# Kernel optimization log

Hardware: AMD Instinct MI355X
Metric: run time of the kernel (lower is better)

## Reference

```python
import jax, jax.numpy as jnp
import numpy as np


def setup_inputs() -> dict:
    key = jax.random.key(0)
    x = jax.random.normal(key, (128, 256, 32, 32), dtype=jnp.float32)
    return {"x": x, "topk": 5}


def reference(x, topk):
    B = x.shape[0]
    flat = x.reshape(B, -1)                      # [B, N]
    _, idx = jax.lax.top_k(flat, topk)           # [B, k] indices into N
    out = jnp.zeros_like(flat)
    out = out.at[jnp.arange(B)[:, None], idx].set(1.0)
    return out.reshape(x.shape)
```

## Files before the change

### kernel.cpp

```cpp
#include <hip/hip_runtime.h>
#include <limits.h>
#include <math.h>
#include <stdint.h>

#define BROWS 128
#define NCOLS (256 * 32 * 32)
#define K 5
#define BPR 16
#define TPB 256
#define CHUNK (NCOLS / BPR)
#define F4T (CHUNK / 4 / TPB)
#define CAP 256

typedef float v4f __attribute__((ext_vector_type(4)));

__device__ __forceinline__ uint64_t make_key(float f, uint32_t idx) {
    uint32_t u = __float_as_uint(f);
    u = (u & 0x80000000u) ? ~u : (u | 0x80000000u);
    return ((uint64_t)u << 32) | (uint32_t)(~idx);
}
__device__ __forceinline__ uint32_t key_idx(uint64_t k) { return ~(uint32_t)k; }

#define KEY_NEG_INF 0x007FFFFF00000000ULL

__device__ __forceinline__ void insert5(uint64_t (&key)[K], uint64_t c) {
    if (c > key[K - 1]) {
        key[K - 1] = c;
#pragma unroll
        for (int s = K - 1; s > 0; --s) {
            if (key[s] > key[s - 1]) {
                uint64_t t = key[s]; key[s] = key[s - 1]; key[s - 1] = t;
            }
        }
    }
}

__device__ __forceinline__ void wave_reduce5(uint64_t (&key)[K]) {
#pragma unroll
    for (int off = 1; off < 64; off <<= 1) {
        uint64_t ok[K];
#pragma unroll
        for (int k = 0; k < K; ++k)
            ok[k] = __shfl_xor((unsigned long long)key[k], off, 64);
#pragma unroll
        for (int k = 0; k < K; ++k) insert5(key, ok[k]);
    }
}

__device__ __forceinline__ void insert5f(float (&v)[K], float c) {
    if (c > v[K - 1]) {
        v[K - 1] = c;
#pragma unroll
        for (int s = K - 1; s > 0; --s) {
            if (v[s] > v[s - 1]) { float t = v[s]; v[s] = v[s - 1]; v[s - 1] = t; }
        }
    }
}

__global__ __launch_bounds__(TPB) void wta_gmax(const float* __restrict__ x,
                                                float* __restrict__ gmax) {
    const int gb = blockIdx.x;
    const float4* __restrict__ x4 = (const float4*)(x + (size_t)gb * CHUNK);
    const int t = threadIdx.x;

    float m = -INFINITY;
#pragma unroll
    for (int i = 0; i < F4T; ++i) {
        const float4 d = x4[t + i * TPB];
        m = fmaxf(m, fmaxf(fmaxf(d.x, d.y), fmaxf(d.z, d.w)));
    }
#pragma unroll
    for (int off = 1; off < 64; off <<= 1)
        m = fmaxf(m, __shfl_xor(m, off, 64));

    __shared__ float sm[TPB / 64];
    if ((t & 63) == 0) sm[t >> 6] = m;
    __syncthreads();
    if (t == 0)
        gmax[gb] = fmaxf(fmaxf(sm[0], sm[1]), fmaxf(sm[2], sm[3]));
}

__global__ __launch_bounds__(64) void wta_thresh(const float* __restrict__ gmax,
                                                 float* __restrict__ T,
                                                 int* __restrict__ cnt) {
    const int row = blockIdx.x, lane = threadIdx.x;
    float v[K];
#pragma unroll
    for (int k = 0; k < K; ++k) v[k] = -INFINITY;
    if (lane < BPR) insert5f(v, gmax[row * BPR + lane]);
#pragma unroll
    for (int off = 1; off < 64; off <<= 1) {
        float ov[K];
#pragma unroll
        for (int k = 0; k < K; ++k) ov[k] = __shfl_xor(v[k], off, 64);
#pragma unroll
        for (int k = 0; k < K; ++k) insert5f(v, ov[k]);
    }
    if (lane == 0) { T[row] = v[K - 1]; cnt[row] = 0; }
}

__global__ __launch_bounds__(TPB) void wta_fillfilter(const float* __restrict__ x,
                                                      float* __restrict__ out,
                                                      const float* __restrict__ T,
                                                      int* __restrict__ cnt,
                                                      uint64_t* __restrict__ cand) {
    const int gb  = blockIdx.x;
    const int row = gb / BPR;
    const int blk = gb % BPR;
    const size_t base = (size_t)gb * CHUNK;
    const float4* __restrict__ x4 = (const float4*)(x + base);
    v4f* __restrict__ o4 = (v4f*)(out + base);
    const int t = threadIdx.x;
    const float Trow = T[row];
    const v4f z = {0.f, 0.f, 0.f, 0.f};

#pragma unroll
    for (int h = 0; h < 2; ++h) {
        float4 r[F4T / 2];
#pragma unroll
        for (int j = 0; j < F4T / 2; ++j)
            r[j] = x4[t + (h * (F4T / 2) + j) * TPB];
#pragma unroll
        for (int j = 0; j < F4T / 2; ++j)
            __builtin_nontemporal_store(z, &o4[t + (h * (F4T / 2) + j) * TPB]);
#pragma unroll
        for (int j = 0; j < F4T / 2; ++j) {
            const float4 d = r[j];
            const float m = fmaxf(fmaxf(d.x, d.y), fmaxf(d.z, d.w));
            if (m >= Trow) {
                const uint32_t e = (uint32_t)blk * CHUNK +
                                   (uint32_t)(t + (h * (F4T / 2) + j) * TPB) * 4u;
                const float vs[4] = {d.x, d.y, d.z, d.w};
#pragma unroll
                for (int c = 0; c < 4; ++c) {
                    if (vs[c] >= Trow) {
                        const int slot = atomicAdd(&cnt[row], 1);
                        if (slot < CAP) cand[row * CAP + slot] = make_key(vs[c], e + c);
                    }
                }
            }
        }
    }
}

__global__ __launch_bounds__(64) void wta_final(const int* __restrict__ cnt,
                                                const uint64_t* __restrict__ cand,
                                                float* __restrict__ out) {
    const int row = blockIdx.x, lane = threadIdx.x;
    const int n = min(cnt[row], CAP);

    uint64_t key[K];
#pragma unroll
    for (int k = 0; k < K; ++k) key[k] = KEY_NEG_INF;
    for (int c = lane; c < n; c += 64) insert5(key, cand[row * CAP + c]);

    wave_reduce5(key);

    if (lane == 0) {
#pragma unroll
        for (int k = 0; k < K; ++k)
            if (key[k] != KEY_NEG_INF)
                out[(size_t)row * NCOLS + key_idx(key[k])] = 1.0f;
    }
}

extern "C" void kernel_launch(void* const* d_in, const int* in_sizes, int n_in,
                              void* d_out, int out_size, void* d_ws, size_t ws_size,
                              hipStream_t stream) {
    const float* x = (const float*)d_in[0];
    float* out = (float*)d_out;

    uint64_t* cand = (uint64_t*)d_ws;
    float* gmax = (float*)(cand + (size_t)BROWS * CAP);
    float* T    = gmax + BROWS * BPR;
    int*   cnt  = (int*)(T + BROWS);

    wta_gmax<<<BROWS * BPR, TPB, 0, stream>>>(x, gmax);
    wta_thresh<<<BROWS, 64, 0, stream>>>(gmax, T, cnt);
    wta_fillfilter<<<BROWS * BPR, TPB, 0, stream>>>(x, out, T, cnt, cand);
    wta_final<<<BROWS, 64, 0, stream>>>(cnt, cand, out);
}
```

Measured before the change: 252.7 us.

## Fuse max prepass into single streaming pass with per-block top-k candidates

Removes the separate global-max and threshold kernels so x is read once instead of twice. Each thread keeps a running top-5 of packed value/index keys and uses its 5th value as a skip threshold. The block reduces this to its own top-5 via wave shuffles and shared memory, and a final kernel merges the 16 per-block lists per row. This trades the atomic candidate buffer for more per-thread insertion work early in the scan.

```diff
diff --git a/kernel.cpp b/kernel.cpp
--- a/kernel.cpp
+++ b/kernel.cpp
@@ -10,7 +10,7 @@
 #define TPB 256
 #define CHUNK (NCOLS / BPR)
 #define F4T (CHUNK / 4 / TPB)
-#define CAP 256
+#define NW (TPB / 64)
 
 typedef float v4f __attribute__((ext_vector_type(4)));
 
@@ -20,6 +20,11 @@
     return ((uint64_t)u << 32) | (uint32_t)(~idx);
 }
 __device__ __forceinline__ uint32_t key_idx(uint64_t k) { return ~(uint32_t)k; }
+__device__ __forceinline__ float key_val(uint64_t k) {
+    uint32_t u = (uint32_t)(k >> 32);
+    u = (u & 0x80000000u) ? (u & 0x7FFFFFFFu) : ~u;
+    return __uint_as_float(u);
+}
 
 #define KEY_NEG_INF 0x007FFFFF00000000ULL
 
@@ -47,63 +52,9 @@
     }
 }
 
-__device__ __forceinline__ void insert5f(float (&v)[K], float c) {
-    if (c > v[K - 1]) {
-        v[K - 1] = c;
-#pragma unroll
-        for (int s = K - 1; s > 0; --s) {
-            if (v[s] > v[s - 1]) { float t = v[s]; v[s] = v[s - 1]; v[s - 1] = t; }
-        }
-    }
-}
-
-__global__ __launch_bounds__(TPB) void wta_gmax(const float* __restrict__ x,
-                                                float* __restrict__ gmax) {
-    const int gb = blockIdx.x;
-    const float4* __restrict__ x4 = (const float4*)(x + (size_t)gb * CHUNK);
-    const int t = threadIdx.x;
-
-    float m = -INFINITY;
-#pragma unroll
-    for (int i = 0; i < F4T; ++i) {
-        const float4 d = x4[t + i * TPB];
-        m = fmaxf(m, fmaxf(fmaxf(d.x, d.y), fmaxf(d.z, d.w)));
-    }
-#pragma unroll
-    for (int off = 1; off < 64; off <<= 1)
-        m = fmaxf(m, __shfl_xor(m, off, 64));
-
-    __shared__ float sm[TPB / 64];
-    if ((t & 63) == 0) sm[t >> 6] = m;
-    __syncthreads();
-    if (t == 0)
-        gmax[gb] = fmaxf(fmaxf(sm[0], sm[1]), fmaxf(sm[2], sm[3]));
-}
-
-__global__ __launch_bounds__(64) void wta_thresh(const float* __restrict__ gmax,
-                                                 float* __restrict__ T,
-                                                 int* __restrict__ cnt) {
-    const int row = blockIdx.x, lane = threadIdx.x;
-    float v[K];
-#pragma unroll
-    for (int k = 0; k < K; ++k) v[k] = -INFINITY;
-    if (lane < BPR) insert5f(v, gmax[row * BPR + lane]);
-#pragma unroll
-    for (int off = 1; off < 64; off <<= 1) {
-        float ov[K];
-#pragma unroll
-        for (int k = 0; k < K; ++k) ov[k] = __shfl_xor(v[k], off, 64);
-#pragma unroll
-        for (int k = 0; k < K; ++k) insert5f(v, ov[k]);
-    }
-    if (lane == 0) { T[row] = v[K - 1]; cnt[row] = 0; }
-}
-
-__global__ __launch_bounds__(TPB) void wta_fillfilter(const float* __restrict__ x,
-                                                      float* __restrict__ out,
-                                                      const float* __restrict__ T,
-                                                      int* __restrict__ cnt,
-                                                      uint64_t* __restrict__ cand) {
+__global__ __launch_bounds__(TPB) void wta_pass(const float* __restrict__ x,
+                                                float* __restrict__ out,
+                                                uint64_t* __restrict__ cand) {
     const int gb  = blockIdx.x;
     const int row = gb / BPR;
     const int blk = gb % BPR;
@@ -111,8 +62,13 @@
     const float4* __restrict__ x4 = (const float4*)(x + base);
     v4f* __restrict__ o4 = (v4f*)(out + base);
     const int t = threadIdx.x;
-    const float Trow = T[row];
     const v4f z = {0.f, 0.f, 0.f, 0.f};
+
+    uint64_t key[K];
+#pragma unroll
+    for (int k = 0; k < K; ++k) key[k] = KEY_NEG_INF;
+    float vth = -INFINITY;
+    const uint32_t ebase = (uint32_t)blk * CHUNK;
 
 #pragma unroll
     for (int h = 0; h < 2; ++h) {
@@ -127,32 +83,52 @@
         for (int j = 0; j < F4T / 2; ++j) {
             const float4 d = r[j];
             const float m = fmaxf(fmaxf(d.x, d.y), fmaxf(d.z, d.w));
-            if (m >= Trow) {
-                const uint32_t e = (uint32_t)blk * CHUNK +
-                                   (uint32_t)(t + (h * (F4T / 2) + j) * TPB) * 4u;
+            if (m >= vth) {
+                const uint32_t e = ebase + (uint32_t)(t + (h * (F4T / 2) + j) * TPB) * 4u;
                 const float vs[4] = {d.x, d.y, d.z, d.w};
 #pragma unroll
-                for (int c = 0; c < 4; ++c) {
-                    if (vs[c] >= Trow) {
-                        const int slot = atomicAdd(&cnt[row], 1);
-                        if (slot < CAP) cand[row * CAP + slot] = make_key(vs[c], e + c);
-                    }
-                }
+                for (int c = 0; c < 4; ++c) insert5(key, make_key(vs[c], e + c));
+                vth = key_val(key[K - 1]);
             }
+        }
+    }
+
+    wave_reduce5(key);
+
+    __shared__ uint64_t sk[NW * K];
+    const int lane = t & 63, w = t >> 6;
+    if (lane == 0) {
+#pragma unroll
+        for (int k = 0; k < K; ++k) sk[w * K + k] = key[k];
+    }
+    __syncthreads();
+    if (t < 64) {
+        uint64_t fk[K];
+#pragma unroll
+        for (int k = 0; k < K; ++k) fk[k] = KEY_NEG_INF;
+        if (t < NW * K) fk[0] = sk[t];
+        wave_reduce5(fk);
+        if (t == 0) {
+#pragma unroll
+            for (int k = 0; k < K; ++k)
+                cand[((size_t)row * BPR + blk) * K + k] = fk[k];
         }
     }
 }
 
-__global__ __launch_bounds__(64) void wta_final(const int* __restrict__ cnt,
-                                                const uint64_t* __restrict__ cand,
+__global__ __launch_bounds__(64) void wta_final(const uint64_t* __restrict__ cand,
                                                 float* __restrict__ out) {
     const int row = blockIdx.x, lane = threadIdx.x;
-    const int n = min(cnt[row], CAP);
+    const uint64_t* __restrict__ c = cand + (size_t)row * BPR * K;
 
     uint64_t key[K];
 #pragma unroll
     for (int k = 0; k < K; ++k) key[k] = KEY_NEG_INF;
-    for (int c = lane; c < n; c += 64) insert5(key, cand[row * CAP + c]);
+#pragma unroll
+    for (int i = 0; i < 2; ++i) {
+        const int j = i * 64 + lane;
+        if (j < BPR * K) insert5(key, c[j]);
+    }
 
     wave_reduce5(key);
 
@@ -171,12 +147,7 @@
     float* out = (float*)d_out;
 
     uint64_t* cand = (uint64_t*)d_ws;
-    float* gmax = (float*)(cand + (size_t)BROWS * CAP);
-    float* T    = gmax + BROWS * BPR;
-    int*   cnt  = (int*)(T + BROWS);
 
-    wta_gmax<<<BROWS * BPR, TPB, 0, stream>>>(x, gmax);
-    wta_thresh<<<BROWS, 64, 0, stream>>>(gmax, T, cnt);
-    wta_fillfilter<<<BROWS * BPR, TPB, 0, stream>>>(x, out, T, cnt, cand);
-    wta_final<<<BROWS, 64, 0, stream>>>(cnt, cand, out);
+    wta_pass<<<BROWS * BPR, TPB, 0, stream>>>(x, out, cand);
+    wta_final<<<BROWS, 64, 0, stream>>>(cand, out);
 }
```

Measured after the change: 264.9 us. 4.8% more time.
